# Kernel tuning notes

Measured on AMD Instinct MI355X. Metric: run time of the kernel, lower is better.

## Reference

```python
import jax, jax.numpy as jnp
import numpy as np

B, W, F_IN = 128, 128, 64   # batch, window_size, num_features
N = 64                      # nodes per graph == num_features == tcn_out_channels
E = 4096                    # edges per graph
ED = 16                     # edge_feature_dim
H, C = 4, 32                # heads, gat_out_dim
FLAT = N * H * C            # 8192
HID = FLAT // 4             # 2048
LRELU_SLOPE = 0.01          # F.leaky_relu default
BN_EPS = 1e-5


def setup_inputs() -> dict:
    key = jax.random.key(0)
    ks = jax.random.split(key, 16)
    x = jax.random.normal(ks[0], (B, W, F_IN), jnp.float32)
    edge_index = jax.random.randint(ks[1], (2, E), 0, N)
    edge_attr = jax.random.normal(ks[2], (B, E, ED), jnp.float32)
    s = lambda k, shape, fan: jax.random.normal(k, shape, jnp.float32) / np.sqrt(fan)
    tcn_w = s(ks[3], (N, F_IN, 3), F_IN * 3)
    tcn_b = jnp.zeros((N,), jnp.float32)
    lin_l_w = s(ks[4], (H * C, W), W)
    lin_l_b = jnp.zeros((H * C,), jnp.float32)
    lin_e_w = s(ks[5], (H * C, ED), ED)
    lin_e_b = jnp.zeros((H * C,), jnp.float32)
    att = s(ks[6], (1, H, C), C)
    fc1_w = s(ks[7], (HID, FLAT), FLAT)
    fc1_b = jnp.zeros((HID,), jnp.float32)
    bn_g = jnp.ones((HID,), jnp.float32)
    bn_b = jnp.zeros((HID,), jnp.float32)
    fc2_w = s(ks[8], (2, HID), HID)
    fc2_b = jnp.zeros((2,), jnp.float32)
    return dict(x=x, edge_index=edge_index, edge_attr=edge_attr,
                tcn_w=tcn_w, tcn_b=tcn_b,
                lin_l_w=lin_l_w, lin_l_b=lin_l_b,
                lin_e_w=lin_e_w, lin_e_b=lin_e_b, att=att,
                fc1_w=fc1_w, fc1_b=fc1_b, bn_g=bn_g, bn_b=bn_b,
                fc2_w=fc2_w, fc2_b=fc2_b)


def reference(x, edge_index, edge_attr, tcn_w, tcn_b,
              lin_l_w, lin_l_b, lin_e_w, lin_e_b, att,
              fc1_w, fc1_b, bn_g, bn_b, fc2_w, fc2_b):
    # TCN: Conv1d(k=3, pad=1) over the window dim
    xt = jnp.transpose(x, (0, 2, 1))  # [B, F_IN, W]
    x_g = jax.lax.conv_general_dilated(
        xt, tcn_w, window_strides=(1,), padding=((1, 1),),
        dimension_numbers=('NCH', 'OIH', 'NCH')) + tcn_b[None, :, None]
    # x_g: [B, N, W] -> per-sample graph with N nodes, W-dim node features

    src, dst = edge_index[0], edge_index[1]

    def gat_one(xn, ea):
        # xn: [N, W], ea: [E, ED]
        h = (xn @ lin_l_w.T + lin_l_b).reshape(N, H, C)
        e = (ea @ lin_e_w.T + lin_e_b).reshape(E, H, C)
        xi = h[dst]               # [E, H, C] target node feats
        xj = h[src]               # [E, H, C] source node feats
        a = jax.nn.leaky_relu(xi + xj + e, LRELU_SLOPE)
        score = jnp.einsum('ehc,ohc->eh', a, att)  # [E, H]
        # segment softmax over edges grouped by destination node
        m = jax.ops.segment_max(score, dst, num_segments=N)
        m = jnp.where(jnp.isfinite(m), m, 0.0)
        ex = jnp.exp(score - m[dst])
        den = jax.ops.segment_sum(ex, dst, num_segments=N)
        alpha = ex / (den[dst] + 1e-16)            # [E, H]
        msg = xj * alpha[:, :, None]               # [E, H, C]
        out = jax.ops.segment_sum(msg, dst, num_segments=N)  # [N, H, C]
        return out.reshape(N, H * C)

    x_gat = jax.vmap(gat_one)(x_g, edge_attr)      # [B, N, H*C]
    x_gat = jax.nn.elu(x_gat)
    x_flat = x_gat.reshape(B, FLAT)

    h1 = x_flat @ fc1_w.T + fc1_b
    # BatchNorm1d in eval mode with fresh running stats (mean=0, var=1)
    h1 = h1 * (bn_g / jnp.sqrt(1.0 + BN_EPS)) + bn_b
    h1 = jax.nn.relu(h1)  # dropout is identity in eval
    logits = h1 @ fc2_w.T + fc2_b
    return logits
```

## Files before the change

kernel.cpp:

```cpp
#include <hip/hip_runtime.h>
#include <math.h>

#define BB   128
#define WW   128
#define FIN  64
#define NNODE 64
#define NE   4096
#define EDIM 16
#define NH   4
#define CDIM 32
#define HC   128
#define FLATD 8192
#define HIDD 2048

#define OFF_H    0u
#define OFF_P    1048576u
#define OFF_XGB  2097152u
#define OFF_BK   2621440u

typedef unsigned short u16;
typedef u16      u16x8 __attribute__((ext_vector_type(8)));
typedef __bf16   bf16x8 __attribute__((ext_vector_type(8)));
typedef float    f32x4  __attribute__((ext_vector_type(4)));
typedef float    f32x16 __attribute__((ext_vector_type(16)));

__device__ __forceinline__ u16 f2bf(float f) {
    unsigned u = __float_as_uint(f);
    u += 0x7fffu + ((u >> 16) & 1u);
    return (u16)(u >> 16);
}
__device__ __forceinline__ void hilo(float v, u16* h, u16* l) {
    u16 hh = f2bf(v);
    float hf = __uint_as_float(((unsigned)hh) << 16);
    *h = hh;
    *l = f2bf(v - hf);
}

__global__ __launch_bounds__(256) void k01(
        const float* __restrict__ x, const float* __restrict__ tcn_w,
        const float* __restrict__ tcn_b, const float* __restrict__ lin_l_w,
        const float* __restrict__ lin_l_b, float* __restrict__ h,
        const int* __restrict__ ei, int* __restrict__ bstart,
        int* __restrict__ blist)
{
    __shared__ float xsw[130*68];
    __shared__ float xg[32*132];
    __shared__ float twn[32*3*68];
    __shared__ int cnt[64];
    __shared__ int cur[65];
    const int bid = blockIdx.x, t = threadIdx.x;

    if (bid == 256) {
        if (t < 64) cnt[t] = 0;
        __syncthreads();
        for (int e = t; e < NE; e += 256) atomicAdd(&cnt[ei[NE + e]], 1);
        __syncthreads();
        if (t == 0) {
            int run = 0;
            for (int n = 0; n < 64; ++n) { cur[n] = run; run += cnt[n]; }
            cur[64] = run;
        }
        __syncthreads();
        if (t < 65) bstart[t] = cur[t];
        __syncthreads();
        for (int e = t; e < NE; e += 256) {
            int d = ei[NE + e], s = ei[e];
            int p = atomicAdd(&cur[d], 1);
            blist[p] = (e << 12) | (d << 6) | s;
        }
        return;
    }

    const int b = bid >> 1, half = bid & 1;
    const int n0 = half * 32;

    for (int idx = t; idx < 8192; idx += 256) {
        const int wo = idx >> 6, i = idx & 63;
        const int row = wo + 1;
        const int g = (row >> 4) & 7;
        xsw[row*68 + (((i >> 2) ^ g) << 2) + (i & 3)] = x[b*8192 + idx];
    }
    for (int idx = t; idx < 6144; idx += 256) {
        const int nl = idx / 192, r = idx - nl*192;
        const int k = r >> 6, i = r & 63;
        twn[(nl*3 + k)*68 + i] = tcn_w[(n0 + nl)*192 + i*3 + k];
    }
    if (t < 68) { xsw[t] = 0.f; xsw[129*68 + t] = 0.f; }
    __syncthreads();

    {
        const int nl = t >> 3;
        const int G  = t & 7;
        const int w0 = G * 16;
        float acc[16];
        const float tb = tcn_b[n0 + nl];
#pragma unroll
        for (int j = 0; j < 16; ++j) acc[j] = tb;
        for (int i4 = 0; i4 < 16; ++i4) {
            const float4 t0v = *(const float4*)&twn[(nl*3 + 0)*68 + i4*4];
            const float4 t1v = *(const float4*)&twn[(nl*3 + 1)*68 + i4*4];
            const float4 t2v = *(const float4*)&twn[(nl*3 + 2)*68 + i4*4];
            float4 r[18];
#pragma unroll
            for (int j = 0; j < 18; ++j) {
                const int gj = (G + (j >= 16 ? 1 : 0)) & 7;
                r[j] = *(const float4*)&xsw[(w0 + j)*68 + ((i4 ^ gj) << 2)];
            }
#pragma unroll
            for (int dw = 0; dw < 16; ++dw) {
                acc[dw] += r[dw+0].x*t0v.x + r[dw+0].y*t0v.y
                         + r[dw+0].z*t0v.z + r[dw+0].w*t0v.w
                         + r[dw+1].x*t1v.x + r[dw+1].y*t1v.y
                         + r[dw+1].z*t1v.z + r[dw+1].w*t1v.w
                         + r[dw+2].x*t2v.x + r[dw+2].y*t2v.y
                         + r[dw+2].z*t2v.z + r[dw+2].w*t2v.w;
            }
        }
#pragma unroll
        for (int dw = 0; dw < 16; ++dw) xg[nl*132 + w0 + dw] = acc[dw];
    }
    __syncthreads();

    {
        const int o2 = t & 63, ng = t >> 6;
        const int oA = o2, oB = o2 + 64;
        float accA[8], accB[8];
        const float lbA = lin_l_b[oA], lbB = lin_l_b[oB];
#pragma unroll
        for (int j = 0; j < 8; ++j) { accA[j] = lbA; accB[j] = lbB; }
        for (int c = 0; c < 32; ++c) {
            const float4 lwA = *(const float4*)&lin_l_w[oA*128 + c*4];
            const float4 lwB = *(const float4*)&lin_l_w[oB*128 + c*4];
#pragma unroll
            for (int nn = 0; nn < 8; ++nn) {
                const float4 xv = *(const float4*)&xg[(ng*8+nn)*132 + c*4];
                accA[nn] += xv.x*lwA.x + xv.y*lwA.y + xv.z*lwA.z + xv.w*lwA.w;
                accB[nn] += xv.x*lwB.x + xv.y*lwB.y + xv.z*lwB.z + xv.w*lwB.w;
            }
        }
#pragma unroll
        for (int nn = 0; nn < 8; ++nn) {
            const int n = n0 + ng*8 + nn;
            h[(b*64 + n)*128 + oA] = accA[nn];
            h[(b*64 + n)*128 + oB] = accB[nn];
        }
    }
}

#define CAPF 2560
__global__ __launch_bounds__(512, 1) void k2_fused(
        const float* __restrict__ hbase, const float* __restrict__ ea,
        const float* __restrict__ lin_e_w, const float* __restrict__ lin_e_b,
        const float* __restrict__ att, const int* __restrict__ bstart,
        const int* __restrict__ blist, u16* __restrict__ xgb)
{
    __shared__ float hbuf[64*132];
    __shared__ float scl[CAPF*4];
    __shared__ float Pm[4][32][68];
    __shared__ int   bst[33];
    const int b = blockIdx.x, half = blockIdx.y, t = threadIdx.x;
    const int lane = t & 63, wv = t >> 6, l32 = lane & 31, h5 = lane >> 5;

    const int lo  = bstart[half*32];
    const int cnt = min(bstart[half*32 + 32] - lo, CAPF);
    const int gcnt = (cnt + 31) >> 5;

    int g = wv;
    int pkc = 0; bool validc = false;
    float4 v0c = {0.f,0.f,0.f,0.f}, v1c = {0.f,0.f,0.f,0.f};
    if (g < gcnt) {
        const int idx0 = g*32 + l32;
        validc = idx0 < cnt;
        pkc = validc ? blist[lo + idx0] : 0;
        const float* eap = ea + ((size_t)b*NE + (size_t)(pkc >> 12))*16 + h5*8;
        v0c = *(const float4*)eap;
        v1c = *(const float4*)(eap + 4);
    }

    for (int idx = t; idx < 2048; idx += 512) {
        const int row = idx >> 5, c4 = (idx & 31) * 4;
        float4 hv = *(const float4*)&hbase[(size_t)b*8192 + row*128 + c4];
        const float4 eb = *(const float4*)&lin_e_b[c4];
        hv.x += 0.5f*eb.x; hv.y += 0.5f*eb.y;
        hv.z += 0.5f*eb.z; hv.w += 0.5f*eb.w;
        *(float4*)&hbuf[row*132 + c4] = hv;
    }
    {
        const f32x4 z4 = {0.f, 0.f, 0.f, 0.f};
        for (int idx = t; idx < 4*32*68/4; idx += 512) ((f32x4*)Pm)[idx] = z4;
    }
    if (t < 33) bst[t] = bstart[half*32 + t];
    bf16x8 Ah[4], Al[4];
#pragma unroll
    for (int mt = 0; mt < 4; ++mt) {
        const float* wp = &lin_e_w[(mt*32 + l32)*16 + h5*8];
        const float4 w0 = *(const float4*)wp;
        const float4 w1 = *(const float4*)(wp + 4);
        u16 th[8], tl[8];
        hilo(w0.x,&th[0],&tl[0]); hilo(w0.y,&th[1],&tl[1]);
        hilo(w0.z,&th[2],&tl[2]); hilo(w0.w,&th[3],&tl[3]);
        hilo(w1.x,&th[4],&tl[4]); hilo(w1.y,&th[5],&tl[5]);
        hilo(w1.z,&th[6],&tl[6]); hilo(w1.w,&th[7],&tl[7]);
        u16x8 vh = { th[0],th[1],th[2],th[3],th[4],th[5],th[6],th[7] };
        u16x8 vl = { tl[0],tl[1],tl[2],tl[3],tl[4],tl[5],tl[6],tl[7] };
        Ah[mt] = *(bf16x8*)&vh;
        Al[mt] = *(bf16x8*)&vl;
    }
    float4 attv[4][4];
#pragma unroll
    for (int mt = 0; mt < 4; ++mt)
#pragma unroll
        for (int gq = 0; gq < 4; ++gq)
            attv[mt][gq] = *(const float4*)&att[mt*32 + gq*8 + h5*4];
    __syncthreads();

    while (g < gcnt) {
        const int gn = g + 8;
        const int pk = pkc; const bool valid = validc;
        const float4 v0 = v0c, v1 = v1c;
        const int idx = g*32 + l32;
        if (gn < gcnt) {
            const int idxn = gn*32 + l32;
            validc = idxn < cnt;
            pkc = validc ? blist[lo + idxn] : 0;
            const float* eap = ea + ((size_t)b*NE + (size_t)(pkc >> 12))*16 + h5*8;
            v0c = *(const float4*)eap;
            v1c = *(const float4*)(eap + 4);
        } else {
            validc = false;
        }
        const int sn = pk & 63, dd = (pk >> 6) & 63;
        u16 bh[8], bl[8];
        hilo(v0.x,&bh[0],&bl[0]); hilo(v0.y,&bh[1],&bl[1]);
        hilo(v0.z,&bh[2],&bl[2]); hilo(v0.w,&bh[3],&bl[3]);
        hilo(v1.x,&bh[4],&bl[4]); hilo(v1.y,&bh[5],&bl[5]);
        hilo(v1.z,&bh[6],&bl[6]); hilo(v1.w,&bh[7],&bl[7]);
        u16x8 vbh = { bh[0],bh[1],bh[2],bh[3],bh[4],bh[5],bh[6],bh[7] };
        u16x8 vbl = { bl[0],bl[1],bl[2],bl[3],bl[4],bl[5],bl[6],bl[7] };
        const bf16x8 Bh = *(bf16x8*)&vbh;
        const bf16x8 Bl = *(bf16x8*)&vbl;
        float hacc[4];
#pragma unroll
        for (int mt = 0; mt < 4; ++mt) {
            f32x16 D = {0.f,0.f,0.f,0.f,0.f,0.f,0.f,0.f,
                        0.f,0.f,0.f,0.f,0.f,0.f,0.f,0.f};
            D = __builtin_amdgcn_mfma_f32_32x32x16_bf16(Al[mt], Bh, D, 0, 0, 0);
            D = __builtin_amdgcn_mfma_f32_32x32x16_bf16(Ah[mt], Bl, D, 0, 0, 0);
            D = __builtin_amdgcn_mfma_f32_32x32x16_bf16(Ah[mt], Bh, D, 0, 0, 0);
            float s = 0.f;
#pragma unroll
            for (int g4 = 0; g4 < 4; ++g4) {
                const int ob = mt*32 + g4*8 + h5*4;
                const float4 hd = *(const float4*)&hbuf[dd*132 + ob];
                const float4 hs = *(const float4*)&hbuf[sn*132 + ob];
                float x0 = hd.x + hs.x + D[g4*4+0];
                float x1 = hd.y + hs.y + D[g4*4+1];
                float x2 = hd.z + hs.z + D[g4*4+2];
                float x3 = hd.w + hs.w + D[g4*4+3];
                x0 = fmaxf(x0, 0.01f*x0); x1 = fmaxf(x1, 0.01f*x1);
                x2 = fmaxf(x2, 0.01f*x2); x3 = fmaxf(x3, 0.01f*x3);
                const float4 a4 = attv[mt][g4];
                s += a4.x*x0 + a4.y*x1 + a4.z*x2 + a4.w*x3;
            }
            hacc[mt] = s;
        }
#pragma unroll
        for (int hh = 0; hh < 4; ++hh)
            hacc[hh] += __shfl_xor(hacc[hh], 32);
        if (h5 == 0 && valid)
            *(float4*)&scl[idx*4] = make_float4(hacc[0], hacc[1], hacc[2], hacc[3]);
        g = gn;
    }
    __syncthreads();

    {
        const int pair = t >> 2, sub = t & 3;
        const int nl = pair >> 2, hh = pair & 3;
        const int s0 = bst[nl] - lo, s1 = bst[nl+1] - lo;
        float mx = -3.4e38f;
        for (int i = s0 + sub; i < s1; i += 4) mx = fmaxf(mx, scl[i*4 + hh]);
        mx = fmaxf(mx, __shfl_xor(mx, 1));
        mx = fmaxf(mx, __shfl_xor(mx, 2));
        float den = 0.f;
        for (int i = s0 + sub; i < s1; i += 4) {
            const float ex = __expf(scl[i*4 + hh] - mx);
            scl[i*4 + hh] = ex;
            den += ex;
        }
        den += __shfl_xor(den, 1);
        den += __shfl_xor(den, 2);
        const float rd = 1.0f / (den + 1e-16f);
        for (int i = s0 + sub; i < s1; i += 4) {
            const int src = blist[lo + i] & 63;
            atomicAdd(&Pm[hh][nl][src], scl[i*4 + hh] * rd);
        }
    }
    __syncthreads();

    {
        const int hh = wv >> 1, ct = wv & 1;
        const int l16 = lane & 15, q = lane >> 4;
        const int cb = hh*32 + ct*16 + l16;
        const float lb2 = 0.5f * lin_e_b[cb];
        bf16x8 Hh2[2], Hl2[2];
#pragma unroll
        for (int kk = 0; kk < 2; ++kk) {
            u16 hhv[8], hlv[8];
#pragma unroll
            for (int i = 0; i < 8; ++i) {
                const float v = hbuf[(kk*32 + q*8 + i)*132 + cb];
                hilo(v, &hhv[i], &hlv[i]);
            }
            u16x8 vhh = { hhv[0],hhv[1],hhv[2],hhv[3],hhv[4],hhv[5],hhv[6],hhv[7] };
            u16x8 vhl = { hlv[0],hlv[1],hlv[2],hlv[3],hlv[4],hlv[5],hlv[6],hlv[7] };
            Hh2[kk] = *(bf16x8*)&vhh;
            Hl2[kk] = *(bf16x8*)&vhl;
        }
#pragma unroll
        for (int mrow = 0; mrow < 32; mrow += 16) {
            f32x4 D = {0.f, 0.f, 0.f, 0.f};
#pragma unroll
            for (int kk = 0; kk < 2; ++kk) {
                const float* pp = &Pm[hh][mrow + l16][kk*32 + q*8];
                const float4 a0 = *(const float4*)pp;
                const float4 a1 = *(const float4*)(pp + 4);
                u16 ph[8], pl[8];
                hilo(a0.x,&ph[0],&pl[0]); hilo(a0.y,&ph[1],&pl[1]);
                hilo(a0.z,&ph[2],&pl[2]); hilo(a0.w,&ph[3],&pl[3]);
                hilo(a1.x,&ph[4],&pl[4]); hilo(a1.y,&ph[5],&pl[5]);
                hilo(a1.z,&ph[6],&pl[6]); hilo(a1.w,&ph[7],&pl[7]);
                u16x8 vph = { ph[0],ph[1],ph[2],ph[3],ph[4],ph[5],ph[6],ph[7] };
                u16x8 vpl = { pl[0],pl[1],pl[2],pl[3],pl[4],pl[5],pl[6],pl[7] };
                const bf16x8 Ph = *(bf16x8*)&vph, Pl = *(bf16x8*)&vpl;
                D = __builtin_amdgcn_mfma_f32_16x16x32_bf16(Pl, Hh2[kk], D, 0, 0, 0);
                D = __builtin_amdgcn_mfma_f32_16x16x32_bf16(Ph, Hl2[kk], D, 0, 0, 0);
                D = __builtin_amdgcn_mfma_f32_16x16x32_bf16(Ph, Hh2[kk], D, 0, 0, 0);
            }
#pragma unroll
            for (int r = 0; r < 4; ++r) {
                const int m = mrow + q*4 + r;
                const float corr = (bst[m+1] > bst[m]) ? lb2 : 0.f;
                float v = D[r] - corr;
                v = v > 0.f ? v : expm1f(v);
                xgb[(size_t)b*8192 + (half*32 + m)*128 + cb] = f2bf(v);
            }
        }
    }
}

#define KTOT 2048
__global__ __launch_bounds__(256) void k3_fc1(
        const u16* __restrict__ xgb, const float* __restrict__ fc1_w,
        float* __restrict__ part)
{
    __shared__ u16 Ash[2][128*72];
    __shared__ u16 Bsh[2][32*72];
    const int jb = blockIdx.x, ks = blockIdx.y, t = threadIdx.x;
    const int j0 = jb*32, k0 = ks*KTOT;
    const int wave = t >> 6, lane = t & 63;
    const int quad = lane >> 4, l16 = lane & 15;
    const int wm = (wave & 1) * 64, wn = (wave >> 1) * 16;

    f32x4 acc[4];
#pragma unroll
    for (int i = 0; i < 4; ++i) acc[i] = (f32x4){0.f, 0.f, 0.f, 0.f};

    const int arow = t >> 1, acol = (t & 1) * 32;
    const int brow = t >> 3, bcol = (t & 7) * 8;

#define K3_LOAD(KC, AR, B0, B1)                                              \
    {   const u16* ap = xgb + (size_t)arow*FLATD + k0 + (KC) + acol;         \
        AR[0] = *(const u16x8*)(ap);      AR[1] = *(const u16x8*)(ap + 8);   \
        AR[2] = *(const u16x8*)(ap + 16); AR[3] = *(const u16x8*)(ap + 24);  \
        const float* bp = fc1_w + (size_t)(j0 + brow)*FLATD + k0 + (KC) + bcol; \
        B0 = *(const float4*)bp; B1 = *(const float4*)(bp + 4); }

#define K3_WRITE(BUF, AR, B0, B1)                                            \
    {   *(u16x8*)&Ash[BUF][arow*72 + acol]      = AR[0];                     \
        *(u16x8*)&Ash[BUF][arow*72 + acol + 8]  = AR[1];                     \
        *(u16x8*)&Ash[BUF][arow*72 + acol + 16] = AR[2];                     \
        *(u16x8*)&Ash[BUF][arow*72 + acol + 24] = AR[3];                     \
        u16x8 u = { f2bf(B0.x), f2bf(B0.y), f2bf(B0.z), f2bf(B0.w),          \
                    f2bf(B1.x), f2bf(B1.y), f2bf(B1.z), f2bf(B1.w) };        \
        *(u16x8*)&Bsh[BUF][brow*72 + bcol] = u; }

#define K3_MFMA(BUF)                                                         \
    {   _Pragma("unroll")                                                    \
        for (int kk = 0; kk < 64; kk += 32) {                                \
            bf16x8 af[4], bfr;                                               \
            _Pragma("unroll")                                                \
            for (int i = 0; i < 4; ++i)                                      \
                af[i] = *(const bf16x8*)&Ash[BUF][(wm + i*16 + l16)*72 + kk + quad*8]; \
            bfr = *(const bf16x8*)&Bsh[BUF][(wn + l16)*72 + kk + quad*8];    \
            _Pragma("unroll")                                                \
            for (int i = 0; i < 4; ++i)                                      \
                acc[i] = __builtin_amdgcn_mfma_f32_16x16x32_bf16(af[i], bfr, acc[i], 0, 0, 0); \
        } }

    u16x8 Ar0[4]; float4 B00, B01;
    u16x8 Ar1[4]; float4 B10, B11;

    K3_LOAD(0, Ar0, B00, B01);
    K3_WRITE(0, Ar0, B00, B01);
    K3_LOAD(64, Ar0, B00, B01);
    K3_LOAD(128, Ar1, B10, B11);
    __syncthreads();

    for (int kc = 0; kc < KTOT; kc += 128) {
        K3_MFMA(0);
        if (kc + 64 < KTOT)  K3_WRITE(1, Ar0, B00, B01);
        if (kc + 192 < KTOT) K3_LOAD(kc + 192, Ar0, B00, B01);
        __syncthreads();
        K3_MFMA(1);
        if (kc + 128 < KTOT) K3_WRITE(0, Ar1, B10, B11);
        if (kc + 256 < KTOT) K3_LOAD(kc + 256, Ar1, B10, B11);
        __syncthreads();
    }
#undef K3_LOAD
#undef K3_WRITE
#undef K3_MFMA

#pragma unroll
    for (int i = 0; i < 4; ++i) {
        const int n = j0 + wn + l16;
#pragma unroll
        for (int r = 0; r < 4; ++r) {
            const int m = wm + i*16 + quad*4 + r;
            part[(size_t)ks*262144 + (size_t)m*HIDD + n] = acc[i][r];
        }
    }
}

__global__ __launch_bounds__(1024) void k4_fc2(
        const float* __restrict__ part, const float* __restrict__ fc1_b,
        const float* __restrict__ bn_g, const float* __restrict__ bn_b,
        const float* __restrict__ fc2_w, const float* __restrict__ fc2_b,
        float* __restrict__ out)
{
    __shared__ float w0s[16], w1s[16];
    const int b = blockIdx.x, t = threadIdx.x;
    const int lane = t & 63, wv = t >> 6;
    const float inv = 1.0f / sqrtf(1.0f + 1e-5f);
    float p0 = 0.f, p1 = 0.f;
#pragma unroll
    for (int jj = 0; jj < 2; ++jj) {
        const int j = t + jj*1024;
        float hv = 0.f;
#pragma unroll
        for (int s = 0; s < 4; ++s) hv += part[(size_t)s*262144 + (size_t)b*2048 + j];
        float v = (hv + fc1_b[j]) * (bn_g[j] * inv) + bn_b[j];
        v = fmaxf(v, 0.f);
        p0 += v * fc2_w[j];
        p1 += v * fc2_w[2048 + j];
    }
#pragma unroll
    for (int d = 1; d < 64; d <<= 1) {
        p0 += __shfl_xor(p0, d);
        p1 += __shfl_xor(p1, d);
    }
    if (lane == 0) { w0s[wv] = p0; w1s[wv] = p1; }
    __syncthreads();
    if (t == 0) {
        float s0 = 0.f, s1 = 0.f;
#pragma unroll
        for (int i = 0; i < 16; ++i) { s0 += w0s[i]; s1 += w1s[i]; }
        out[b*2 + 0] = s0 + fc2_b[0];
        out[b*2 + 1] = s1 + fc2_b[1];
    }
}

extern "C" void kernel_launch(void* const* d_in, const int* in_sizes, int n_in,
                              void* d_out, int out_size, void* d_ws, size_t ws_size,
                              hipStream_t stream)
{
    const float* x       = (const float*)d_in[0];
    const int*   ei      = (const int*)  d_in[1];
    const float* ea      = (const float*)d_in[2];
    const float* tcn_w   = (const float*)d_in[3];
    const float* tcn_b   = (const float*)d_in[4];
    const float* lin_l_w = (const float*)d_in[5];
    const float* lin_l_b = (const float*)d_in[6];
    const float* lin_e_w = (const float*)d_in[7];
    const float* lin_e_b = (const float*)d_in[8];
    const float* att     = (const float*)d_in[9];
    const float* fc1_w   = (const float*)d_in[10];
    const float* fc1_b   = (const float*)d_in[11];
    const float* bn_g    = (const float*)d_in[12];
    const float* bn_b    = (const float*)d_in[13];
    const float* fc2_w   = (const float*)d_in[14];
    const float* fc2_b   = (const float*)d_in[15];

    float* ws     = (float*)d_ws;
    float* hbuf   = ws + OFF_H;
    float* part   = ws + OFF_P;
    u16*   xgb    = (u16*)(ws + OFF_XGB);
    int*   bstart = (int*)(ws + OFF_BK);
    int*   blist  = bstart + 80;
    float* out    = (float*)d_out;

    k01     <<<257, 256, 0, stream>>>(x, tcn_w, tcn_b, lin_l_w, lin_l_b, hbuf,
                                      ei, bstart, blist);
    k2_fused<<<dim3(BB, 2), 512, 0, stream>>>(hbuf, ea, lin_e_w, lin_e_b, att,
                                              bstart, blist, xgb);
    k3_fc1  <<<dim3(64, 4), 256, 0, stream>>>(xgb, fc1_w, part);
    k4_fc2  <<<BB, 1024, 0, stream>>>(part, fc1_b, bn_g, bn_b, fc2_w, fc2_b, out);
}
```

Measured before the change: 223.7 us.

## Fuse BN/ReLU/fc2 epilogue into fc1 GEMM, drop split-K partials

The fc1 GEMM no longer splits K. It now runs 128 blocks, each owning 16 hidden columns across the full K of 8192. The bias, batch-norm, ReLU and fc2 dot product are applied in its epilogue, and per-row results are reduced with shuffles plus atomicAdd into a small accumulator that k01 zeroes. This removes the large partial-sum buffer write and read and replaces the 1024-thread fc2 kernel with a trivial output kernel. The cost is a lower MFMA tile per wave and fewer blocks doing more serial K-iterations, which can leave the GPU underoccupied and expose memory latency. Float atomics also make the summation order nondeterministic.

```diff
diff --git a/kernel.cpp b/kernel.cpp
--- a/kernel.cpp
+++ b/kernel.cpp
@@ -14,9 +14,9 @@
 #define HIDD 2048
 
 #define OFF_H    0u
-#define OFF_P    1048576u
-#define OFF_XGB  2097152u
-#define OFF_BK   2621440u
+#define OFF_XGB  1048576u
+#define OFF_ACC  1572864u
+#define OFF_BK   1573120u
 
 typedef unsigned short u16;
 typedef u16      u16x8 __attribute__((ext_vector_type(8)));
@@ -41,7 +41,7 @@
         const float* __restrict__ tcn_b, const float* __restrict__ lin_l_w,
         const float* __restrict__ lin_l_b, float* __restrict__ h,
         const int* __restrict__ ei, int* __restrict__ bstart,
-        int* __restrict__ blist)
+        int* __restrict__ blist, float* __restrict__ accbuf)
 {
     __shared__ float xsw[130*68];
     __shared__ float xg[32*132];
@@ -51,6 +51,7 @@
     const int bid = blockIdx.x, t = threadIdx.x;
 
     if (bid == 256) {
+        accbuf[t] = 0.f;
         if (t < 64) cnt[t] = 0;
         __syncthreads();
         for (int e = t; e < NE; e += 256) atomicAdd(&cnt[ei[NE + e]], 1);
@@ -348,57 +349,52 @@
     }
 }
 
-#define KTOT 2048
-__global__ __launch_bounds__(256) void k3_fc1(
+#define KTOT 8192
+__global__ __launch_bounds__(512) void k3_fc1(
         const u16* __restrict__ xgb, const float* __restrict__ fc1_w,
-        float* __restrict__ part)
+        const float* __restrict__ fc1_b, const float* __restrict__ bn_g,
+        const float* __restrict__ bn_b, const float* __restrict__ fc2_w,
+        float* __restrict__ accbuf)
 {
     __shared__ u16 Ash[2][128*72];
-    __shared__ u16 Bsh[2][32*72];
-    const int jb = blockIdx.x, ks = blockIdx.y, t = threadIdx.x;
-    const int j0 = jb*32, k0 = ks*KTOT;
+    __shared__ u16 Bsh[2][16*72];
+    const int jb = blockIdx.x, t = threadIdx.x;
+    const int j0 = jb*16;
     const int wave = t >> 6, lane = t & 63;
     const int quad = lane >> 4, l16 = lane & 15;
-    const int wm = (wave & 1) * 64, wn = (wave >> 1) * 16;
-
-    f32x4 acc[4];
-#pragma unroll
-    for (int i = 0; i < 4; ++i) acc[i] = (f32x4){0.f, 0.f, 0.f, 0.f};
-
-    const int arow = t >> 1, acol = (t & 1) * 32;
+
+    f32x4 acc = (f32x4){0.f, 0.f, 0.f, 0.f};
+
+    const int arow = t >> 2, acol = (t & 3) * 16;
     const int brow = t >> 3, bcol = (t & 7) * 8;
 
-#define K3_LOAD(KC, AR, B0, B1)                                              \
-    {   const u16* ap = xgb + (size_t)arow*FLATD + k0 + (KC) + acol;         \
-        AR[0] = *(const u16x8*)(ap);      AR[1] = *(const u16x8*)(ap + 8);   \
-        AR[2] = *(const u16x8*)(ap + 16); AR[3] = *(const u16x8*)(ap + 24);  \
-        const float* bp = fc1_w + (size_t)(j0 + brow)*FLATD + k0 + (KC) + bcol; \
-        B0 = *(const float4*)bp; B1 = *(const float4*)(bp + 4); }
-
-#define K3_WRITE(BUF, AR, B0, B1)                                            \
-    {   *(u16x8*)&Ash[BUF][arow*72 + acol]      = AR[0];                     \
-        *(u16x8*)&Ash[BUF][arow*72 + acol + 8]  = AR[1];                     \
-        *(u16x8*)&Ash[BUF][arow*72 + acol + 16] = AR[2];                     \
-        *(u16x8*)&Ash[BUF][arow*72 + acol + 24] = AR[3];                     \
-        u16x8 u = { f2bf(B0.x), f2bf(B0.y), f2bf(B0.z), f2bf(B0.w),          \
-                    f2bf(B1.x), f2bf(B1.y), f2bf(B1.z), f2bf(B1.w) };        \
-        *(u16x8*)&Bsh[BUF][brow*72 + bcol] = u; }
-
-#define K3_MFMA(BUF)                                                         \
-    {   _Pragma("unroll")                                                    \
-        for (int kk = 0; kk < 64; kk += 32) {                                \
-            bf16x8 af[4], bfr;                                               \
-            _Pragma("unroll")                                                \
-            for (int i = 0; i < 4; ++i)                                      \
-                af[i] = *(const bf16x8*)&Ash[BUF][(wm + i*16 + l16)*72 + kk + quad*8]; \
-            bfr = *(const bf16x8*)&Bsh[BUF][(wn + l16)*72 + kk + quad*8];    \
-            _Pragma("unroll")                                                \
-            for (int i = 0; i < 4; ++i)                                      \
-                acc[i] = __builtin_amdgcn_mfma_f32_16x16x32_bf16(af[i], bfr, acc[i], 0, 0, 0); \
+#define K3_LOAD(KC, AR, B0, B1)                                               \
+    {   const u16* ap = xgb + (size_t)arow*FLATD + (KC) + acol;               \
+        AR[0] = *(const u16x8*)(ap); AR[1] = *(const u16x8*)(ap + 8);         \
+        if (t < 128) {                                                        \
+            const float* bp = fc1_w + (size_t)(j0 + brow)*FLATD + (KC) + bcol;\
+            B0 = *(const float4*)bp; B1 = *(const float4*)(bp + 4);           \
         } }
 
-    u16x8 Ar0[4]; float4 B00, B01;
-    u16x8 Ar1[4]; float4 B10, B11;
+#define K3_WRITE(BUF, AR, B0, B1)                                             \
+    {   *(u16x8*)&Ash[BUF][arow*72 + acol]     = AR[0];                       \
+        *(u16x8*)&Ash[BUF][arow*72 + acol + 8] = AR[1];                       \
+        if (t < 128) {                                                        \
+            u16x8 u = { f2bf(B0.x), f2bf(B0.y), f2bf(B0.z), f2bf(B0.w),       \
+                        f2bf(B1.x), f2bf(B1.y), f2bf(B1.z), f2bf(B1.w) };     \
+            *(u16x8*)&Bsh[BUF][brow*72 + bcol] = u;                           \
+        } }
+
+#define K3_MFMA(BUF)                                                          \
+    {   _Pragma("unroll")                                                     \
+        for (int kk = 0; kk < 64; kk += 32) {                                 \
+            bf16x8 af = *(const bf16x8*)&Ash[BUF][(wave*16 + l16)*72 + kk + quad*8]; \
+            bf16x8 bf = *(const bf16x8*)&Bsh[BUF][l16*72 + kk + quad*8];      \
+            acc = __builtin_amdgcn_mfma_f32_16x16x32_bf16(af, bf, acc, 0, 0, 0); \
+        } }
+
+    u16x8 Ar0[2]; float4 B00 = {0,0,0,0}, B01 = {0,0,0,0};
+    u16x8 Ar1[2]; float4 B10 = {0,0,0,0}, B11 = {0,0,0,0};
 
     K3_LOAD(0, Ar0, B00, B01);
     K3_WRITE(0, Ar0, B00, B01);
@@ -420,53 +416,35 @@
 #undef K3_WRITE
 #undef K3_MFMA
 
-#pragma unroll
-    for (int i = 0; i < 4; ++i) {
-        const int n = j0 + wn + l16;
+    {
+        const float inv = 1.0f / sqrtf(1.0f + 1e-5f);
+        const int n = j0 + l16;
+        const float gj = bn_g[n] * inv, bj = bn_b[n], fj = fc1_b[n];
+        const float w0 = fc2_w[n], w1 = fc2_w[2048 + n];
 #pragma unroll
         for (int r = 0; r < 4; ++r) {
-            const int m = wm + i*16 + quad*4 + r;
-            part[(size_t)ks*262144 + (size_t)m*HIDD + n] = acc[i][r];
-        }
-    }
-}
-
-__global__ __launch_bounds__(1024) void k4_fc2(
-        const float* __restrict__ part, const float* __restrict__ fc1_b,
-        const float* __restrict__ bn_g, const float* __restrict__ bn_b,
-        const float* __restrict__ fc2_w, const float* __restrict__ fc2_b,
+            float v = (acc[r] + fj) * gj + bj;
+            v = fmaxf(v, 0.f);
+            float q0 = v * w0, q1 = v * w1;
+            q0 += __shfl_xor(q0, 1); q1 += __shfl_xor(q1, 1);
+            q0 += __shfl_xor(q0, 2); q1 += __shfl_xor(q1, 2);
+            q0 += __shfl_xor(q0, 4); q1 += __shfl_xor(q1, 4);
+            q0 += __shfl_xor(q0, 8); q1 += __shfl_xor(q1, 8);
+            if (l16 == 0) {
+                const int m = wave*16 + quad*4 + r;
+                atomicAdd(&accbuf[m*2 + 0], q0);
+                atomicAdd(&accbuf[m*2 + 1], q1);
+            }
+        }
+    }
+}
+
+__global__ __launch_bounds__(256) void k4_out(
+        const float* __restrict__ accbuf, const float* __restrict__ fc2_b,
         float* __restrict__ out)
 {
-    __shared__ float w0s[16], w1s[16];
-    const int b = blockIdx.x, t = threadIdx.x;
-    const int lane = t & 63, wv = t >> 6;
-    const float inv = 1.0f / sqrtf(1.0f + 1e-5f);
-    float p0 = 0.f, p1 = 0.f;
-#pragma unroll
-    for (int jj = 0; jj < 2; ++jj) {
-        const int j = t + jj*1024;
-        float hv = 0.f;
-#pragma unroll
-        for (int s = 0; s < 4; ++s) hv += part[(size_t)s*262144 + (size_t)b*2048 + j];
-        float v = (hv + fc1_b[j]) * (bn_g[j] * inv) + bn_b[j];
-        v = fmaxf(v, 0.f);
-        p0 += v * fc2_w[j];
-        p1 += v * fc2_w[2048 + j];
-    }
-#pragma unroll
-    for (int d = 1; d < 64; d <<= 1) {
-        p0 += __shfl_xor(p0, d);
-        p1 += __shfl_xor(p1, d);
-    }
-    if (lane == 0) { w0s[wv] = p0; w1s[wv] = p1; }
-    __syncthreads();
-    if (t == 0) {
-        float s0 = 0.f, s1 = 0.f;
-#pragma unroll
-        for (int i = 0; i < 16; ++i) { s0 += w0s[i]; s1 += w1s[i]; }
-        out[b*2 + 0] = s0 + fc2_b[0];
-        out[b*2 + 1] = s1 + fc2_b[1];
-    }
+    const int t = threadIdx.x;
+    out[t] = accbuf[t] + fc2_b[t & 1];
 }
 
 extern "C" void kernel_launch(void* const* d_in, const int* in_sizes, int n_in,
@@ -492,16 +470,17 @@
 
     float* ws     = (float*)d_ws;
     float* hbuf   = ws + OFF_H;
-    float* part   = ws + OFF_P;
     u16*   xgb    = (u16*)(ws + OFF_XGB);
+    float* accbuf = ws + OFF_ACC;
     int*   bstart = (int*)(ws + OFF_BK);
     int*   blist  = bstart + 80;
     float* out    = (float*)d_out;
 
     k01     <<<257, 256, 0, stream>>>(x, tcn_w, tcn_b, lin_l_w, lin_l_b, hbuf,
-                                      ei, bstart, blist);
+                                      ei, bstart, blist, accbuf);
     k2_fused<<<dim3(BB, 2), 512, 0, stream>>>(hbuf, ea, lin_e_w, lin_e_b, att,
                                               bstart, blist, xgb);
-    k3_fc1  <<<dim3(64, 4), 256, 0, stream>>>(xgb, fc1_w, part);
-    k4_fc2  <<<BB, 1024, 0, stream>>>(part, fc1_b, bn_g, bn_b, fc2_w, fc2_b, out);
-}
+    k3_fc1  <<<128, 512, 0, stream>>>(xgb, fc1_w, fc1_b, bn_g, bn_b, fc2_w,
+                                      accbuf);
+    k4_out  <<<1, 256, 0, stream>>>(accbuf, fc2_b, out);
+}
```

Result: slower. 285.0 us (+27.4%).
